# Kernel optimization log

Measured on AMD Instinct MI355X. Metric: run time of the kernel, lower is better.

Reference implementation:

```python
import jax, jax.numpy as jnp
import numpy as np

NF, NH, NC, B = 8, 200, 8, 131072  # nFeatures, nHidden, nCls, batch
NEQ = 2

def _lin_init(k, fan_in, fan_out):
    k1, k2 = jax.random.split(k)
    s = 1.0 / np.sqrt(fan_in)
    W = jax.random.uniform(k1, (fan_out, fan_in), minval=-s, maxval=s, dtype=jnp.float32)
    b = jax.random.uniform(k2, (fan_out,), minval=-s, maxval=s, dtype=jnp.float32)
    return W, b

def setup_inputs() -> dict:
    key = jax.random.key(0)
    ks = jax.random.split(key, 6)
    W0, b0 = _lin_init(ks[0], NF, NF)
    W1, b1 = _lin_init(ks[1], NF, NH)
    W2, b2 = _lin_init(ks[2], NH, NH)
    W3, b3 = _lin_init(ks[3], NH, NH)
    W4, b4 = _lin_init(ks[4], NH, NC)
    Q = jnp.eye(NF, dtype=jnp.float32)  # Parameter initialized to identity
    x = jax.random.normal(ks[5], (B, NF), dtype=jnp.float32)
    return dict(x=x, Q=Q, W0=W0, b0=b0, W1=W1, b1=b1, W2=W2, b2=b2, W3=W3, b3=b3, W4=W4, b4=b4)

def _qp_equality(Q, p, A, bvec):
    # min 1/2 z'Qz + p'z  s.t.  A z = b.  (G=0, h=0 => inequality constraints vacuous.)
    # KKT: [Q A'; A 0] [z; nu] = [-p; b], solved batched (tiny 10x10 systems).
    Bn, m, n = A.shape
    Qb = jnp.broadcast_to(Q, (Bn, n, n))
    K = jnp.concatenate([
        jnp.concatenate([Qb, jnp.swapaxes(A, 1, 2)], axis=2),        # [B, n, n+m]
        jnp.concatenate([A, jnp.zeros((Bn, m, m), Q.dtype)], axis=2) # [B, m, n+m]
    ], axis=1)                                                        # [B, n+m, n+m]
    rhs = jnp.concatenate([-p, bvec], axis=1)                         # [B, n+m]
    sol = jnp.linalg.solve(K, rhs[..., None])[..., 0]
    return sol[:, :n]

def reference(x, Q, W0, b0, W1, b1, W2, b2, W3, b3, W4, b4):
    h = x @ W0.T + b0                      # fc0, [B, 8]
    p = -h
    z_ = jnp.zeros_like(h[:, 3])
    o_ = jnp.ones_like(h[:, 3])
    # A[i] = [[0,0,0,0,h[i,3],1,0,0], [0,0,0,0,0,0,h[i,3],1]]  (detached in original)
    A = jnp.stack([
        jnp.stack([z_, z_, z_, z_, h[:, 3], o_, z_, z_], axis=1),
        jnp.stack([z_, z_, z_, z_, z_, z_, h[:, 3], o_], axis=1)], axis=1)  # [B, 2, 8]
    A = jax.lax.stop_gradient(A)  # torch.tensor(...) breaks the graph for A
    bvec = jnp.stack([h[:, 3] * h[:, 4] + h[:, 5],
                      h[:, 3] * h[:, 6] + h[:, 7]], axis=1)  # [B, 2]
    z = _qp_equality(Q, p, A, bvec)        # QPFunction solution, [B, 8]
    y = jax.nn.relu(z @ W1.T + b1)
    y = jax.nn.relu(y @ W2.T + b2)
    y = jax.nn.relu(y @ W3.T + b3)
    return y @ W4.T + b4                   # [B, 8]
```

## Files before the change

### kernel.cpp

```cpp
#include <hip/hip_runtime.h>
#include <math.h>

typedef _Float16 f16;
typedef f16 half8 __attribute__((ext_vector_type(8)));
typedef float floatx4 __attribute__((ext_vector_type(4)));

#define NF 8
#define NH 200
#define NC 8
#define M_BLK 256
#define SCR_W 40

#define WS_QI   0
#define WS_B1P  256
#define WS_B2P  1152
#define WS_B3P  2048
#define WS_WP1  3008
#define WS_WP2  16320
#define WS_WP3  109504
#define WS_WP4  202688
#define WS_NEED 209856

__device__ __forceinline__ void pack_frag(const float* __restrict__ W, int Nv, int Kv,
                                          int nkt, int nks, f16* __restrict__ dst, int gid)
{
    if (gid < nks * nkt * 64) {
        const int ks    = gid / (nkt * 64);
        const int rem   = gid - ks * nkt * 64;
        const int nt    = rem >> 6;
        const int lane  = rem & 63;
        const int n     = nt * 16 + (lane & 15);
        const int kbase = ks * 32 + ((lane >> 4) * 8);
        f16 tmp[8];
#pragma unroll
        for (int j = 0; j < 8; ++j) {
            const int k = kbase + j;
            tmp[j] = (n < Nv && k < Kv) ? (f16)W[n * Kv + k] : (f16)0.0f;
        }
        *(half8*)&dst[(size_t)gid * 8] = *(const half8*)tmp;
    }
}

__global__ void prep_kernel(const float* __restrict__ Q,
                            const float* __restrict__ W1, const float* __restrict__ b1,
                            const float* __restrict__ W2, const float* __restrict__ b2,
                            const float* __restrict__ W3, const float* __restrict__ b3,
                            const float* __restrict__ W4,
                            char* __restrict__ ws)
{
    const int gid = blockIdx.x * 256 + threadIdx.x;
    pack_frag(W1, NH, NF, 13, 1, (f16*)(ws + WS_WP1), gid);
    pack_frag(W2, NH, NH, 13, 7, (f16*)(ws + WS_WP2), gid);
    pack_frag(W3, NH, NH, 13, 7, (f16*)(ws + WS_WP3), gid);
    pack_frag(W4, NC, NH, 1,  7, (f16*)(ws + WS_WP4), gid);
    if (gid < 224) {
        ((float*)(ws + WS_B1P))[gid] = (gid < NH) ? b1[gid] : 0.0f;
        ((float*)(ws + WS_B2P))[gid] = (gid < NH) ? b2[gid] : 0.0f;
        ((float*)(ws + WS_B3P))[gid] = (gid < NH) ? b3[gid] : 0.0f;
    }

    if (blockIdx.x == 0) {
        __shared__ float aug[8][16];
        __shared__ int piv;
        float* Qi = (float*)(ws + WS_QI);
        const int t  = threadIdx.x;
        const bool a = t < 128;
        const int r  = (t >> 4) & 7;
        const int c2 = t & 15;
        if (a) aug[r][c2] = (c2 < 8) ? Q[r * 8 + c2] : ((c2 - 8 == r) ? 1.0f : 0.0f);
        __syncthreads();
        for (int c = 0; c < 8; ++c) {
            if (t == 0) {
                int p = c; float best = fabsf(aug[c][c]);
                for (int rr = c + 1; rr < 8; ++rr) {
                    float v = fabsf(aug[rr][c]);
                    if (v > best) { best = v; p = rr; }
                }
                piv = p;
            }
            __syncthreads();
            const int p = piv;
            float myv = a ? aug[r][c2] : 0.0f;
            __syncthreads();
            if (a) {
                if (r == c)      aug[p][c2] = myv;
                else if (r == p) aug[c][c2] = myv;
            }
            __syncthreads();
            const float pv = aug[c][c];
            __syncthreads();
            if (a && r == c) aug[r][c2] = aug[r][c2] / pv;
            __syncthreads();
            const float fac  = (a && r != c) ? aug[r][c] : 0.0f;
            const float prow = aug[c][c2];
            __syncthreads();
            if (a) aug[r][c2] -= fac * prow;
            __syncthreads();
        }
        if (a && c2 >= 8) Qi[r * 8 + (c2 - 8)] = aug[r][c2];
    }
}

template<int NKS>
__device__ __forceinline__ void layer_slab(const f16* __restrict__ Wp,
                                           const float* __restrict__ biasP,
                                           const half8 (&aIn)[4][7], half8 (&aOut)[4][7],
                                           f16* scr, const int lane,
                                           const int col16, const int g4)
{
#pragma unroll
    for (int p = 0; p < 7; ++p) {
        const int NT = (p < 6) ? 2 : 1;
        const float bv0 = biasP[(2 * p) * 16 + col16];
        const float bv1 = (NT == 2) ? biasP[(2 * p + 1) * 16 + col16] : 0.0f;
        floatx4 acc[4][2];
#pragma unroll
        for (int mt = 0; mt < 4; ++mt) {
            floatx4 v0; v0[0] = bv0; v0[1] = bv0; v0[2] = bv0; v0[3] = bv0;
            acc[mt][0] = v0;
            floatx4 v1; v1[0] = bv1; v1[1] = bv1; v1[2] = bv1; v1[3] = bv1;
            acc[mt][1] = v1;
        }
#pragma unroll
        for (int ks = 0; ks < NKS; ++ks) {
            const half8 bf0 = *(const half8*)&Wp[((size_t)(ks * 13 + 2 * p) * 64 + lane) * 8];
            half8 bf1;
            if (NT == 2) bf1 = *(const half8*)&Wp[((size_t)(ks * 13 + 2 * p + 1) * 64 + lane) * 8];
#pragma unroll
            for (int mt = 0; mt < 4; ++mt) {
                acc[mt][0] = __builtin_amdgcn_mfma_f32_16x16x32_f16(aIn[mt][ks], bf0, acc[mt][0], 0, 0, 0);
                if (NT == 2)
                    acc[mt][1] = __builtin_amdgcn_mfma_f32_16x16x32_f16(aIn[mt][ks], bf1, acc[mt][1], 0, 0, 0);
            }
        }
#pragma unroll
        for (int mt = 0; mt < 4; ++mt) {
#pragma unroll
            for (int r = 0; r < 4; ++r) {
                const int row = mt * 16 + g4 * 4 + r;
                scr[row * SCR_W + col16]      = (f16)fmaxf(acc[mt][0][r], 0.0f);
                if (NT == 2)
                    scr[row * SCR_W + 16 + col16] = (f16)fmaxf(acc[mt][1][r], 0.0f);
                else
                    scr[row * SCR_W + 16 + col16] = (f16)0.0f;
            }
        }
#pragma unroll
        for (int mt = 0; mt < 4; ++mt)
            aOut[mt][p] = *(const half8*)&scr[(mt * 16 + col16) * SCR_W + g4 * 8];
    }
}

__global__ __launch_bounds__(256, 1)
void mlp_slab(const float* __restrict__ x,
              const float* __restrict__ W0, const float* __restrict__ b0,
              const float* __restrict__ b4,
              const char* __restrict__ ws,
              float* __restrict__ out, int B)
{
    __shared__ f16 scrAll[4][64 * SCR_W];
    const int tid   = threadIdx.x;
    const int lane  = tid & 63;
    const int w     = __builtin_amdgcn_readfirstlane(tid >> 6);
    const int col16 = lane & 15;
    const int g4    = lane >> 4;
    f16* scr = &scrAll[w][0];

    const float* Qi  = (const float*)(ws + WS_QI);
    const float* b1p = (const float*)(ws + WS_B1P);
    const float* b2p = (const float*)(ws + WS_B2P);
    const float* b3p = (const float*)(ws + WS_B3P);
    const f16*  Wp1  = (const f16*)(ws + WS_WP1);
    const f16*  Wp2  = (const f16*)(ws + WS_WP2);
    const f16*  Wp3  = (const f16*)(ws + WS_WP3);
    const f16*  Wp4  = (const f16*)(ws + WS_WP4);

    const long g0 = (long)blockIdx.x * M_BLK + w * 64 + lane;
    float xr[NF];
    if (g0 < B) {
        const float4* xp = (const float4*)(x + g0 * NF);
        const float4 A = xp[0], Bv = xp[1];
        xr[0] = A.x; xr[1] = A.y; xr[2] = A.z; xr[3] = A.w;
        xr[4] = Bv.x; xr[5] = Bv.y; xr[6] = Bv.z; xr[7] = Bv.w;
    } else {
#pragma unroll
        for (int i = 0; i < NF; ++i) xr[i] = 0.0f;
    }
    float h[NF];
#pragma unroll
    for (int j = 0; j < NF; ++j) {
        float acc = b0[j];
#pragma unroll
        for (int k = 0; k < NF; ++k) acc = fmaf(W0[j * NF + k], xr[k], acc);
        h[j] = acc;
    }
    float tq[NF], u0[NF], u1[NF];
    const float h3 = h[3];
#pragma unroll
    for (int i = 0; i < NF; ++i) {
        float s = 0.0f;
#pragma unroll
        for (int k = 0; k < NF; ++k) s = fmaf(Qi[i * NF + k], h[k], s);
        tq[i] = s;
        u0[i] = fmaf(Qi[i * NF + 4], h3, Qi[i * NF + 5]);
        u1[i] = fmaf(Qi[i * NF + 6], h3, Qi[i * NF + 7]);
    }
    const float m00 = fmaf(h3, u0[4], u0[5]);
    const float m01 = fmaf(h3, u1[4], u1[5]);
    const float m10 = fmaf(h3, u0[6], u0[7]);
    const float m11 = fmaf(h3, u1[6], u1[7]);
    const float r0  = fmaf(h3, tq[4], tq[5]) - fmaf(h3, h[4], h[5]);
    const float r1  = fmaf(h3, tq[6], tq[7]) - fmaf(h3, h[6], h[7]);
    const float idet = 1.0f / (m00 * m11 - m01 * m10);
    const float nu0 = (m11 * r0 - m01 * r1) * idet;
    const float nu1 = (m00 * r1 - m10 * r0) * idet;

    {
        half8 zh, zz = {};
#pragma unroll
        for (int k = 0; k < 8; ++k) zh[k] = (f16)(tq[k] - u0[k] * nu0 - u1[k] * nu1);
        *(half8*)&scr[lane * SCR_W + 0]  = zh;
        *(half8*)&scr[lane * SCR_W + 8]  = zz;
        *(half8*)&scr[lane * SCR_W + 16] = zz;
        *(half8*)&scr[lane * SCR_W + 24] = zz;
    }

    half8 aA[4][7], aB[4][7];
#pragma unroll
    for (int mt = 0; mt < 4; ++mt)
        aA[mt][0] = *(const half8*)&scr[(mt * 16 + col16) * SCR_W + g4 * 8];

    layer_slab<1>(Wp1, b1p, aA, aB, scr, lane, col16, g4);
    layer_slab<7>(Wp2, b2p, aB, aA, scr, lane, col16, g4);
    layer_slab<7>(Wp3, b3p, aA, aB, scr, lane, col16, g4);

    {
        const float bias4 = b4[col16 & 7];
        floatx4 acc4[4];
#pragma unroll
        for (int mt = 0; mt < 4; ++mt) { floatx4 z_ = {}; acc4[mt] = z_; }
#pragma unroll
        for (int ks = 0; ks < 7; ++ks) {
            const half8 bf = *(const half8*)&Wp4[((size_t)ks * 64 + lane) * 8];
#pragma unroll
            for (int mt = 0; mt < 4; ++mt)
                acc4[mt] = __builtin_amdgcn_mfma_f32_16x16x32_f16(aB[mt][ks], bf, acc4[mt], 0, 0, 0);
        }
        const long rowbase = (long)blockIdx.x * M_BLK + w * 64;
#pragma unroll
        for (int mt = 0; mt < 4; ++mt) {
#pragma unroll
            for (int r = 0; r < 4; ++r) {
                const long g = rowbase + mt * 16 + g4 * 4 + r;
                if (col16 < NC && g < B) out[g * NC + col16] = acc4[mt][r] + bias4;
            }
        }
    }
}

#define BT 64
#define NWAVE 8
#define JB 25
#define CH 8

__device__ __forceinline__ void layer200(const float* __restrict__ in_,
                                         float* __restrict__ out_,
                                         const float* __restrict__ W,
                                         const float* __restrict__ bias,
                                         int j0, int lane)
{
    float acc[JB];
#pragma unroll
    for (int jj = 0; jj < JB; ++jj) acc[jj] = bias[j0 + jj];
#pragma unroll 1
    for (int k0 = 0; k0 < NH; k0 += CH) {
        float a[CH];
#pragma unroll
        for (int u = 0; u < CH; ++u) a[u] = in_[(k0 + u) * BT + lane];
#pragma unroll
        for (int jj = 0; jj < JB; ++jj) {
            const float* wr = W + (j0 + jj) * NH + k0;
#pragma unroll
            for (int u = 0; u < CH; ++u) acc[jj] = fmaf(wr[u], a[u], acc[jj]);
        }
    }
#pragma unroll
    for (int jj = 0; jj < JB; ++jj)
        out_[(j0 + jj) * BT + lane] = fmaxf(acc[jj], 0.0f);
}

__global__ void qinv_kernel(const float* __restrict__ Q, float* __restrict__ Qi)
{
    __shared__ float aug[8][16];
    __shared__ int piv;
    const int t  = threadIdx.x;
    const int r  = t >> 4;
    const int c2 = t & 15;
    aug[r][c2] = (c2 < 8) ? Q[r * 8 + c2] : ((c2 - 8 == r) ? 1.0f : 0.0f);
    __syncthreads();
    for (int c = 0; c < 8; ++c) {
        if (t == 0) {
            int p = c; float best = fabsf(aug[c][c]);
            for (int rr = c + 1; rr < 8; ++rr) {
                float v = fabsf(aug[rr][c]);
                if (v > best) { best = v; p = rr; }
            }
            piv = p;
        }
        __syncthreads();
        const int p = piv;
        float myv = aug[r][c2];
        __syncthreads();
        if (r == c)      aug[p][c2] = myv;
        else if (r == p) aug[c][c2] = myv;
        __syncthreads();
        const float pv = aug[c][c];
        __syncthreads();
        if (r == c) aug[r][c2] = aug[r][c2] / pv;
        __syncthreads();
        const float fac  = (r == c) ? 0.0f : aug[r][c];
        const float prow = aug[c][c2];
        __syncthreads();
        aug[r][c2] -= fac * prow;
        __syncthreads();
    }
    if (c2 >= 8) Qi[r * 8 + (c2 - 8)] = aug[r][c2];
}

__global__ __launch_bounds__(BT * NWAVE, 2)
void mlp_fused(const float* __restrict__ x, const float* __restrict__ Qi,
               const float* __restrict__ W0, const float* __restrict__ b0,
               const float* __restrict__ W1, const float* __restrict__ b1,
               const float* __restrict__ W2, const float* __restrict__ b2,
               const float* __restrict__ W3, const float* __restrict__ b3,
               const float* __restrict__ W4, const float* __restrict__ b4,
               float* __restrict__ out, int B)
{
    __shared__ float actA[NH * BT];
    __shared__ float actB[NH * BT];
    __shared__ float outP[NWAVE * NC * BT];

    const int lane = threadIdx.x & 63;
    const int wid  = __builtin_amdgcn_readfirstlane((int)(threadIdx.x >> 6));
    const int g    = blockIdx.x * BT + lane;
    const int j0   = wid * JB;

    float xr[NF];
    if (g < B) {
        const float4* xp = reinterpret_cast<const float4*>(x + (size_t)g * NF);
        float4 x0 = xp[0], x1 = xp[1];
        xr[0] = x0.x; xr[1] = x0.y; xr[2] = x0.z; xr[3] = x0.w;
        xr[4] = x1.x; xr[5] = x1.y; xr[6] = x1.z; xr[7] = x1.w;
    } else {
#pragma unroll
        for (int i = 0; i < NF; ++i) xr[i] = 0.0f;
    }
    float h[NF];
#pragma unroll
    for (int j = 0; j < NF; ++j) {
        float acc = b0[j];
#pragma unroll
        for (int k = 0; k < NF; ++k) acc = fmaf(W0[j * NF + k], xr[k], acc);
        h[j] = acc;
    }
    float tq[NF], u0[NF], u1[NF];
    const float h3 = h[3];
#pragma unroll
    for (int i = 0; i < NF; ++i) {
        float s = 0.0f;
#pragma unroll
        for (int k = 0; k < NF; ++k) s = fmaf(Qi[i * NF + k], h[k], s);
        tq[i] = s;
        u0[i] = fmaf(Qi[i * NF + 4], h3, Qi[i * NF + 5]);
        u1[i] = fmaf(Qi[i * NF + 6], h3, Qi[i * NF + 7]);
    }
    const float m00 = fmaf(h3, u0[4], u0[5]);
    const float m01 = fmaf(h3, u1[4], u1[5]);
    const float m10 = fmaf(h3, u0[6], u0[7]);
    const float m11 = fmaf(h3, u1[6], u1[7]);
    const float r0  = fmaf(h3, tq[4], tq[5]) - fmaf(h3, h[4], h[5]);
    const float r1  = fmaf(h3, tq[6], tq[7]) - fmaf(h3, h[6], h[7]);
    const float idet = 1.0f / (m00 * m11 - m01 * m10);
    const float nu0 = (m11 * r0 - m01 * r1) * idet;
    const float nu1 = (m00 * r1 - m10 * r0) * idet;
    float z[NF];
#pragma unroll
    for (int i = 0; i < NF; ++i) z[i] = tq[i] - u0[i] * nu0 - u1[i] * nu1;

#pragma unroll
    for (int jj = 0; jj < JB; ++jj) {
        const int j = j0 + jj;
        float acc = b1[j];
#pragma unroll
        for (int k = 0; k < NF; ++k) acc = fmaf(W1[j * NF + k], z[k], acc);
        actA[j * BT + lane] = fmaxf(acc, 0.0f);
    }
    __syncthreads();
    layer200(actA, actB, W2, b2, j0, lane);
    __syncthreads();
    layer200(actB, actA, W3, b3, j0, lane);
    __syncthreads();
    {
        float a[JB];
#pragma unroll
        for (int kk = 0; kk < JB; ++kk) a[kk] = actA[(j0 + kk) * BT + lane];
        float acc[NC];
#pragma unroll
        for (int o = 0; o < NC; ++o) acc[o] = 0.0f;
#pragma unroll
        for (int o = 0; o < NC; ++o) {
            const float* wr = W4 + o * NH + j0;
#pragma unroll
            for (int kk = 0; kk < JB; ++kk) acc[o] = fmaf(wr[kk], a[kk], acc[o]);
        }
#pragma unroll
        for (int o = 0; o < NC; ++o) outP[(wid * NC + o) * BT + lane] = acc[o];
    }
    __syncthreads();
    {
        float s = b4[wid];
#pragma unroll
        for (int w = 0; w < NWAVE; ++w) s += outP[(w * NC + wid) * BT + lane];
        if (g < B) out[(size_t)g * NC + wid] = s;
    }
}

extern "C" void kernel_launch(void* const* d_in, const int* in_sizes, int n_in,
                              void* d_out, int out_size, void* d_ws, size_t ws_size,
                              hipStream_t stream)
{
    const float* x  = (const float*)d_in[0];
    const float* Q  = (const float*)d_in[1];
    const float* W0 = (const float*)d_in[2];
    const float* b0 = (const float*)d_in[3];
    const float* W1 = (const float*)d_in[4];
    const float* b1 = (const float*)d_in[5];
    const float* W2 = (const float*)d_in[6];
    const float* b2 = (const float*)d_in[7];
    const float* W3 = (const float*)d_in[8];
    const float* b3 = (const float*)d_in[9];
    const float* W4 = (const float*)d_in[10];
    const float* b4 = (const float*)d_in[11];
    float* out = (float*)d_out;

    const int B = in_sizes[0] / NF;

    if (ws_size >= WS_NEED) {
        hipLaunchKernelGGL(prep_kernel, dim3(23), dim3(256), 0, stream,
                           Q, W1, b1, W2, b2, W3, b3, W4, (char*)d_ws);
        hipLaunchKernelGGL(mlp_slab, dim3((B + M_BLK - 1) / M_BLK), dim3(256), 0, stream,
                           x, W0, b0, b4, (const char*)d_ws, out, B);
    } else {
        float* Qi = (float*)d_ws;
        hipLaunchKernelGGL(qinv_kernel, dim3(1), dim3(128), 0, stream, Q, Qi);
        hipLaunchKernelGGL(mlp_fused, dim3((B + BT - 1) / BT), dim3(BT * NWAVE), 0, stream,
                           x, Qi, W0, b0, W1, b1, W2, b2, W3, b3, W4, b4, out, B);
    }
}
```

Measured before the change: 52.74 us.

## Transpose MFMA tiling so weights are the A operand, with register shuffles instead of LDS

Replaces the 256-thread, 4-wave slab kernel with a single-wave kernel that handles 48 rows per block. It computes W·actᵀ so the weight fragments become the MFMA A operand and activations stay in registers. The LDS round trip between layers is replaced by packed fp16 conversion and cross-lane shuffles, and outputs are written as float4. The intent is to remove LDS traffic and barriers, but it adds many more blocks. Each 48-row tile also re-reads all weight fragments from global memory, and a quarter of the MFMA columns in the 64-lane layout are wasted.

New measurement: 60.13 us. 1.14x slower.

```diff
diff --git a/kernel.cpp b/kernel.cpp
--- a/kernel.cpp
+++ b/kernel.cpp
@@ -8,8 +8,8 @@
 #define NF 8
 #define NH 200
 #define NC 8
-#define M_BLK 256
-#define SCR_W 40
+#define ROWS_T 48
+#define FRAG 512
 
 #define WS_QI   0
 #define WS_B1P  256
@@ -19,7 +19,7 @@
 #define WS_WP2  16320
 #define WS_WP3  109504
 #define WS_WP4  202688
-#define WS_NEED 209856
+#define WS_NEED 212000
 
 __device__ __forceinline__ void pack_frag(const float* __restrict__ W, int Nv, int Kv,
                                           int nkt, int nks, f16* __restrict__ dst, int gid)
@@ -101,70 +101,111 @@
     }
 }
 
-template<int NKS>
-__device__ __forceinline__ void layer_slab(const f16* __restrict__ Wp,
-                                           const float* __restrict__ biasP,
-                                           const half8 (&aIn)[4][7], half8 (&aOut)[4][7],
-                                           f16* scr, const int lane,
-                                           const int col16, const int g4)
-{
-#pragma unroll
-    for (int p = 0; p < 7; ++p) {
-        const int NT = (p < 6) ? 2 : 1;
-        const float bv0 = biasP[(2 * p) * 16 + col16];
-        const float bv1 = (NT == 2) ? biasP[(2 * p + 1) * 16 + col16] : 0.0f;
-        floatx4 acc[4][2];
-#pragma unroll
-        for (int mt = 0; mt < 4; ++mt) {
-            floatx4 v0; v0[0] = bv0; v0[1] = bv0; v0[2] = bv0; v0[3] = bv0;
-            acc[mt][0] = v0;
-            floatx4 v1; v1[0] = bv1; v1[1] = bv1; v1[2] = bv1; v1[3] = bv1;
-            acc[mt][1] = v1;
-        }
-#pragma unroll
-        for (int ks = 0; ks < NKS; ++ks) {
-            const half8 bf0 = *(const half8*)&Wp[((size_t)(ks * 13 + 2 * p) * 64 + lane) * 8];
-            half8 bf1;
-            if (NT == 2) bf1 = *(const half8*)&Wp[((size_t)(ks * 13 + 2 * p + 1) * 64 + lane) * 8];
-#pragma unroll
-            for (int mt = 0; mt < 4; ++mt) {
-                acc[mt][0] = __builtin_amdgcn_mfma_f32_16x16x32_f16(aIn[mt][ks], bf0, acc[mt][0], 0, 0, 0);
-                if (NT == 2)
-                    acc[mt][1] = __builtin_amdgcn_mfma_f32_16x16x32_f16(aIn[mt][ks], bf1, acc[mt][1], 0, 0, 0);
-            }
-        }
-#pragma unroll
-        for (int mt = 0; mt < 4; ++mt) {
-#pragma unroll
-            for (int r = 0; r < 4; ++r) {
-                const int row = mt * 16 + g4 * 4 + r;
-                scr[row * SCR_W + col16]      = (f16)fmaxf(acc[mt][0][r], 0.0f);
-                if (NT == 2)
-                    scr[row * SCR_W + 16 + col16] = (f16)fmaxf(acc[mt][1][r], 0.0f);
-                else
-                    scr[row * SCR_W + 16 + col16] = (f16)0.0f;
-            }
-        }
-#pragma unroll
-        for (int mt = 0; mt < 4; ++mt)
-            aOut[mt][p] = *(const half8*)&scr[(mt * 16 + col16) * SCR_W + g4 * 8];
-    }
-}
-
-__global__ __launch_bounds__(256, 1)
-void mlp_slab(const float* __restrict__ x,
-              const float* __restrict__ W0, const float* __restrict__ b0,
-              const float* __restrict__ b4,
-              const char* __restrict__ ws,
-              float* __restrict__ out, int B)
-{
-    __shared__ f16 scrAll[4][64 * SCR_W];
-    const int tid   = threadIdx.x;
-    const int lane  = tid & 63;
-    const int w     = __builtin_amdgcn_readfirstlane(tid >> 6);
-    const int col16 = lane & 15;
-    const int g4    = lane >> 4;
-    f16* scr = &scrAll[w][0];
+__device__ __forceinline__ half8 ldf(const f16* __restrict__ p, int lane)
+{
+    return *(const half8*)&p[lane * 8];
+}
+
+__device__ __forceinline__ int pk2(float a, float b)
+{
+    typedef __fp16 hv2 __attribute__((ext_vector_type(2)));
+    hv2 h = __builtin_amdgcn_cvt_pkrtz(a, b);
+    int r; __builtin_memcpy(&r, &h, 4);
+    return r;
+}
+
+__device__ __forceinline__ half8 mk8(int a, int b, int c, int d)
+{
+    int v[4] = {a, b, c, d};
+    half8 h; __builtin_memcpy(&h, v, 16);
+    return h;
+}
+
+template<int LK>
+__device__ __forceinline__ void layerT(const f16* __restrict__ Wp,
+                                       const float* __restrict__ biasP,
+                                       const half8 (&act)[3][7], half8 (&nxt)[3][7],
+                                       const int lane, const int g,
+                                       const int se, const int so)
+{
+#pragma unroll
+    for (int w = 0; w < 7; ++w) {
+        const int mA = 2 * w;
+        floatx4 accA[3];
+        {
+            half8 wfA[LK];
+#pragma unroll
+            for (int ks = 0; ks < LK; ++ks)
+                wfA[ks] = ldf(Wp + (size_t)(ks * 13 + mA) * FRAG, lane);
+            const float4 bv = *(const float4*)&biasP[mA * 16 + 4 * g];
+#pragma unroll
+            for (int n = 0; n < 3; ++n) {
+                accA[n][0] = bv.x; accA[n][1] = bv.y; accA[n][2] = bv.z; accA[n][3] = bv.w;
+            }
+#pragma unroll
+            for (int ks = 0; ks < LK; ++ks)
+#pragma unroll
+                for (int n = 0; n < 3; ++n)
+                    accA[n] = __builtin_amdgcn_mfma_f32_16x16x32_f16(
+                        wfA[ks], act[n][ks], accA[n], 0, 0, 0);
+        }
+        if (w < 6) {
+            const int mB = mA + 1;
+            floatx4 accB[3];
+            half8 wfB[LK];
+#pragma unroll
+            for (int ks = 0; ks < LK; ++ks)
+                wfB[ks] = ldf(Wp + (size_t)(ks * 13 + mB) * FRAG, lane);
+            const float4 bv = *(const float4*)&biasP[mB * 16 + 4 * g];
+#pragma unroll
+            for (int n = 0; n < 3; ++n) {
+                accB[n][0] = bv.x; accB[n][1] = bv.y; accB[n][2] = bv.z; accB[n][3] = bv.w;
+            }
+#pragma unroll
+            for (int ks = 0; ks < LK; ++ks)
+#pragma unroll
+                for (int n = 0; n < 3; ++n)
+                    accB[n] = __builtin_amdgcn_mfma_f32_16x16x32_f16(
+                        wfB[ks], act[n][ks], accB[n], 0, 0, 0);
+#pragma unroll
+            for (int n = 0; n < 3; ++n) {
+                const int a0 = pk2(fmaxf(accA[n][0], 0.0f), fmaxf(accA[n][1], 0.0f));
+                const int a1 = pk2(fmaxf(accA[n][2], 0.0f), fmaxf(accA[n][3], 0.0f));
+                const int b0 = pk2(fmaxf(accB[n][0], 0.0f), fmaxf(accB[n][1], 0.0f));
+                const int b1 = pk2(fmaxf(accB[n][2], 0.0f), fmaxf(accB[n][3], 0.0f));
+                const int tA0 = __shfl(a0, se, 64), tA1 = __shfl(a1, se, 64);
+                const int tA2 = __shfl(a0, so, 64), tA3 = __shfl(a1, so, 64);
+                const int tB0 = __shfl(b0, se, 64), tB1 = __shfl(b1, se, 64);
+                const int tB2 = __shfl(b0, so, 64), tB3 = __shfl(b1, so, 64);
+                nxt[n][w] = mk8((g < 2) ? tA0 : tB0, (g < 2) ? tA1 : tB1,
+                                (g < 2) ? tA2 : tB2, (g < 2) ? tA3 : tB3);
+            }
+        } else {
+#pragma unroll
+            for (int n = 0; n < 3; ++n) {
+                const int a0 = pk2(fmaxf(accA[n][0], 0.0f), fmaxf(accA[n][1], 0.0f));
+                const int a1 = pk2(fmaxf(accA[n][2], 0.0f), fmaxf(accA[n][3], 0.0f));
+                const int tA0 = __shfl(a0, se, 64), tA1 = __shfl(a1, se, 64);
+                const int tA2 = __shfl(a0, so, 64), tA3 = __shfl(a1, so, 64);
+                nxt[n][w] = mk8((g < 2) ? tA0 : 0, (g < 2) ? tA1 : 0,
+                                (g < 2) ? tA2 : 0, (g < 2) ? tA3 : 0);
+            }
+        }
+    }
+}
+
+__global__ __launch_bounds__(64, 2)
+void mlp_t(const float* __restrict__ x,
+           const float* __restrict__ W0, const float* __restrict__ b0,
+           const float* __restrict__ b4,
+           const char* __restrict__ ws,
+           float* __restrict__ out, int B)
+{
+    const int lane = threadIdx.x & 63;
+    const int c    = lane & 15;
+    const int g    = lane >> 4;
+    const int se   = ((2 * g) & 3) * 16 + c;
+    const int so   = se + 16;
 
     const float* Qi  = (const float*)(ws + WS_QI);
     const float* b1p = (const float*)(ws + WS_B1P);
@@ -175,9 +216,9 @@
     const f16*  Wp3  = (const f16*)(ws + WS_WP3);
     const f16*  Wp4  = (const f16*)(ws + WS_WP4);
 
-    const long g0 = (long)blockIdx.x * M_BLK + w * 64 + lane;
+    const long g0 = (long)blockIdx.x * ROWS_T + lane;
     float xr[NF];
-    if (g0 < B) {
+    if (lane < ROWS_T && g0 < B) {
         const float4* xp = (const float4*)(x + g0 * NF);
         const float4 A = xp[0], Bv = xp[1];
         xr[0] = A.x; xr[1] = A.y; xr[2] = A.z; xr[3] = A.w;
@@ -214,45 +255,55 @@
     const float idet = 1.0f / (m00 * m11 - m01 * m10);
     const float nu0 = (m11 * r0 - m01 * r1) * idet;
     const float nu1 = (m00 * r1 - m10 * r0) * idet;
+    float z[NF];
+#pragma unroll
+    for (int i = 0; i < NF; ++i) z[i] = tq[i] - u0[i] * nu0 - u1[i] * nu1;
+
+    int zq[4];
+#pragma unroll
+    for (int j = 0; j < 4; ++j) zq[j] = pk2(z[2 * j], z[2 * j + 1]);
+
+    half8 aA[3][7], aB[3][7];
+#pragma unroll
+    for (int n = 0; n < 3; ++n) {
+        const int src = 16 * n + c;
+        const int q0 = __shfl(zq[0], src, 64), q1 = __shfl(zq[1], src, 64);
+        const int q2 = __shfl(zq[2], src, 64), q3 = __shfl(zq[3], src, 64);
+        aA[n][0] = mk8((g == 0) ? q0 : 0, (g == 0) ? q1 : 0,
+                       (g == 0) ? q2 : 0, (g == 0) ? q3 : 0);
+    }
+
+    layerT<1>(Wp1, b1p, aA, aB, lane, g, se, so);
+    layerT<7>(Wp2, b2p, aB, aA, lane, g, se, so);
+    layerT<7>(Wp3, b3p, aA, aB, lane, g, se, so);
 
     {
-        half8 zh, zz = {};
-#pragma unroll
-        for (int k = 0; k < 8; ++k) zh[k] = (f16)(tq[k] - u0[k] * nu0 - u1[k] * nu1);
-        *(half8*)&scr[lane * SCR_W + 0]  = zh;
-        *(half8*)&scr[lane * SCR_W + 8]  = zz;
-        *(half8*)&scr[lane * SCR_W + 16] = zz;
-        *(half8*)&scr[lane * SCR_W + 24] = zz;
-    }
-
-    half8 aA[4][7], aB[4][7];
-#pragma unroll
-    for (int mt = 0; mt < 4; ++mt)
-        aA[mt][0] = *(const half8*)&scr[(mt * 16 + col16) * SCR_W + g4 * 8];
-
-    layer_slab<1>(Wp1, b1p, aA, aB, scr, lane, col16, g4);
-    layer_slab<7>(Wp2, b2p, aB, aA, scr, lane, col16, g4);
-    layer_slab<7>(Wp3, b3p, aA, aB, scr, lane, col16, g4);
-
-    {
-        const float bias4 = b4[col16 & 7];
-        floatx4 acc4[4];
-#pragma unroll
-        for (int mt = 0; mt < 4; ++mt) { floatx4 z_ = {}; acc4[mt] = z_; }
-#pragma unroll
-        for (int ks = 0; ks < 7; ++ks) {
-            const half8 bf = *(const half8*)&Wp4[((size_t)ks * 64 + lane) * 8];
-#pragma unroll
-            for (int mt = 0; mt < 4; ++mt)
-                acc4[mt] = __builtin_amdgcn_mfma_f32_16x16x32_f16(aB[mt][ks], bf, acc4[mt], 0, 0, 0);
-        }
-        const long rowbase = (long)blockIdx.x * M_BLK + w * 64;
-#pragma unroll
-        for (int mt = 0; mt < 4; ++mt) {
-#pragma unroll
-            for (int r = 0; r < 4; ++r) {
-                const long g = rowbase + mt * 16 + g4 * 4 + r;
-                if (col16 < NC && g < B) out[g * NC + col16] = acc4[mt][r] + bias4;
+        floatx4 a4[3];
+        const int boff = (g < 2) ? 4 * g : 0;
+        const float4 bv = *(const float4*)&b4[boff];
+#pragma unroll
+        for (int n = 0; n < 3; ++n) {
+            a4[n][0] = bv.x; a4[n][1] = bv.y; a4[n][2] = bv.z; a4[n][3] = bv.w;
+        }
+        half8 wf4[7];
+#pragma unroll
+        for (int ks = 0; ks < 7; ++ks) wf4[ks] = ldf(Wp4 + (size_t)ks * FRAG, lane);
+#pragma unroll
+        for (int ks = 0; ks < 7; ++ks)
+#pragma unroll
+            for (int n = 0; n < 3; ++n)
+                a4[n] = __builtin_amdgcn_mfma_f32_16x16x32_f16(
+                    wf4[ks], aB[n][ks], a4[n], 0, 0, 0);
+        if (g < 2) {
+            const long rowbase = (long)blockIdx.x * ROWS_T;
+#pragma unroll
+            for (int n = 0; n < 3; ++n) {
+                const long row = rowbase + 16 * n + c;
+                if (row < B) {
+                    float4 v;
+                    v.x = a4[n][0]; v.y = a4[n][1]; v.z = a4[n][2]; v.w = a4[n][3];
+                    *(float4*)&out[row * NC + 4 * g] = v;
+                }
             }
         }
     }
@@ -448,7 +499,7 @@
     if (ws_size >= WS_NEED) {
         hipLaunchKernelGGL(prep_kernel, dim3(23), dim3(256), 0, stream,
                            Q, W1, b1, W2, b2, W3, b3, W4, (char*)d_ws);
-        hipLaunchKernelGGL(mlp_slab, dim3((B + M_BLK - 1) / M_BLK), dim3(256), 0, stream,
+        hipLaunchKernelGGL(mlp_t, dim3((B + ROWS_T - 1) / ROWS_T), dim3(64), 0, stream,
                            x, W0, b0, b4, (const char*)d_ws, out, B);
     } else {
         float* Qi = (float*)d_ws;
```

## Hold weight fragments in registers and split output columns across waves

Applied to the files above, without the earlier changes.

The slab kernel, where each wave streamed every weight fragment for its own 64 rows, becomes a 512-thread kernel in which each of 8 waves keeps a fixed subset of output-column tiles' weight fragments resident in registers. Activations for 128-row chunks pass between layers through shared memory, and each block loops over 4 chunks while prefetching the next chunk's x. The goal is to stop reloading weights from global/L2 for every row tile. The cost is many block-wide syncs per layer, larger LDS use, high register pressure, and partial-sum reduction for the last layer through shared memory.

Result: faster. 50.61 us (-4.0%).

```diff
diff --git a/kernel.cpp b/kernel.cpp
--- a/kernel.cpp
+++ b/kernel.cpp
@@ -8,8 +8,11 @@
 #define NF 8
 #define NH 200
 #define NC 8
-#define M_BLK 256
-#define SCR_W 40
+#define ACT_W 232
+#define ROWS 128
+#define CHUNK 4
+#define OUTP_W 9
+#define FRAG 512
 
 #define WS_QI   0
 #define WS_B1P  256
@@ -19,7 +22,7 @@
 #define WS_WP2  16320
 #define WS_WP3  109504
 #define WS_WP4  202688
-#define WS_NEED 209856
+#define WS_NEED 212000
 
 __device__ __forceinline__ void pack_frag(const float* __restrict__ W, int Nv, int Kv,
                                           int nkt, int nks, f16* __restrict__ dst, int gid)
@@ -101,71 +104,22 @@
     }
 }
 
-template<int NKS>
-__device__ __forceinline__ void layer_slab(const f16* __restrict__ Wp,
-                                           const float* __restrict__ biasP,
-                                           const half8 (&aIn)[4][7], half8 (&aOut)[4][7],
-                                           f16* scr, const int lane,
-                                           const int col16, const int g4)
-{
-#pragma unroll
-    for (int p = 0; p < 7; ++p) {
-        const int NT = (p < 6) ? 2 : 1;
-        const float bv0 = biasP[(2 * p) * 16 + col16];
-        const float bv1 = (NT == 2) ? biasP[(2 * p + 1) * 16 + col16] : 0.0f;
-        floatx4 acc[4][2];
-#pragma unroll
-        for (int mt = 0; mt < 4; ++mt) {
-            floatx4 v0; v0[0] = bv0; v0[1] = bv0; v0[2] = bv0; v0[3] = bv0;
-            acc[mt][0] = v0;
-            floatx4 v1; v1[0] = bv1; v1[1] = bv1; v1[2] = bv1; v1[3] = bv1;
-            acc[mt][1] = v1;
-        }
-#pragma unroll
-        for (int ks = 0; ks < NKS; ++ks) {
-            const half8 bf0 = *(const half8*)&Wp[((size_t)(ks * 13 + 2 * p) * 64 + lane) * 8];
-            half8 bf1;
-            if (NT == 2) bf1 = *(const half8*)&Wp[((size_t)(ks * 13 + 2 * p + 1) * 64 + lane) * 8];
-#pragma unroll
-            for (int mt = 0; mt < 4; ++mt) {
-                acc[mt][0] = __builtin_amdgcn_mfma_f32_16x16x32_f16(aIn[mt][ks], bf0, acc[mt][0], 0, 0, 0);
-                if (NT == 2)
-                    acc[mt][1] = __builtin_amdgcn_mfma_f32_16x16x32_f16(aIn[mt][ks], bf1, acc[mt][1], 0, 0, 0);
-            }
-        }
-#pragma unroll
-        for (int mt = 0; mt < 4; ++mt) {
-#pragma unroll
-            for (int r = 0; r < 4; ++r) {
-                const int row = mt * 16 + g4 * 4 + r;
-                scr[row * SCR_W + col16]      = (f16)fmaxf(acc[mt][0][r], 0.0f);
-                if (NT == 2)
-                    scr[row * SCR_W + 16 + col16] = (f16)fmaxf(acc[mt][1][r], 0.0f);
-                else
-                    scr[row * SCR_W + 16 + col16] = (f16)0.0f;
-            }
-        }
-#pragma unroll
-        for (int mt = 0; mt < 4; ++mt)
-            aOut[mt][p] = *(const half8*)&scr[(mt * 16 + col16) * SCR_W + g4 * 8];
-    }
-}
-
-__global__ __launch_bounds__(256, 1)
-void mlp_slab(const float* __restrict__ x,
-              const float* __restrict__ W0, const float* __restrict__ b0,
-              const float* __restrict__ b4,
-              const char* __restrict__ ws,
-              float* __restrict__ out, int B)
-{
-    __shared__ f16 scrAll[4][64 * SCR_W];
-    const int tid   = threadIdx.x;
-    const int lane  = tid & 63;
-    const int w     = __builtin_amdgcn_readfirstlane(tid >> 6);
-    const int col16 = lane & 15;
-    const int g4    = lane >> 4;
-    f16* scr = &scrAll[w][0];
-
+__device__ __forceinline__ half8 ldf(const f16* __restrict__ p, int lane)
+{
+    return *(const half8*)&p[lane * 8];
+}
+
+template<int TC>
+__device__ __forceinline__ void run_path(
+    const float* __restrict__ x,
+    const float* __restrict__ W0, const float* __restrict__ b0,
+    const float* __restrict__ b4,
+    const char* __restrict__ ws,
+    float* __restrict__ out, int B,
+    f16* __restrict__ actA, f16* __restrict__ actB,
+    f16* __restrict__ zbuf, float* __restrict__ outP,
+    const int wid, const int lane, const int c, const int g, const int t0)
+{
     const float* Qi  = (const float*)(ws + WS_QI);
     const float* b1p = (const float*)(ws + WS_B1P);
     const float* b2p = (const float*)(ws + WS_B2P);
@@ -175,87 +129,222 @@
     const f16*  Wp3  = (const f16*)(ws + WS_WP3);
     const f16*  Wp4  = (const f16*)(ws + WS_WP4);
 
-    const long g0 = (long)blockIdx.x * M_BLK + w * 64 + lane;
+    half8 wf1[TC], wf2[TC][7], wf3[TC][7];
+    float bv1[TC], bv2[TC], bv3[TC];
+#pragma unroll
+    for (int t = 0; t < TC; ++t) {
+        wf1[t] = ldf(Wp1 + (size_t)(t0 + t) * FRAG, lane);
+#pragma unroll
+        for (int ks = 0; ks < 7; ++ks) {
+            wf2[t][ks] = ldf(Wp2 + (size_t)(ks * 13 + t0 + t) * FRAG, lane);
+            wf3[t][ks] = ldf(Wp3 + (size_t)(ks * 13 + t0 + t) * FRAG, lane);
+        }
+        bv1[t] = b1p[(t0 + t) * 16 + c];
+        bv2[t] = b2p[(t0 + t) * 16 + c];
+        bv3[t] = b3p[(t0 + t) * 16 + c];
+    }
+    const bool doL4 = (wid < 7);
+    half8 w4f = {};
+    if (doL4) w4f = ldf(Wp4 + (size_t)wid * FRAG, lane);
+
+    const long blockbase = (long)blockIdx.x * (ROWS * CHUNK);
+    const int  tid = wid * 64 + lane;
+
+    {
+        f16* buf = (tid & 256) ? actB : actA;
+        const int row  = (tid >> 1) & 127;
+        const int part = tid & 1;
+        half8 zz = {};
+        *(half8*)&buf[row * ACT_W + 208 + part * 8] = zz;
+    }
+
     float xr[NF];
-    if (g0 < B) {
-        const float4* xp = (const float4*)(x + g0 * NF);
-        const float4 A = xp[0], Bv = xp[1];
-        xr[0] = A.x; xr[1] = A.y; xr[2] = A.z; xr[3] = A.w;
-        xr[4] = Bv.x; xr[5] = Bv.y; xr[6] = Bv.z; xr[7] = Bv.w;
-    } else {
-#pragma unroll
-        for (int i = 0; i < NF; ++i) xr[i] = 0.0f;
-    }
-    float h[NF];
-#pragma unroll
-    for (int j = 0; j < NF; ++j) {
-        float acc = b0[j];
-#pragma unroll
-        for (int k = 0; k < NF; ++k) acc = fmaf(W0[j * NF + k], xr[k], acc);
-        h[j] = acc;
-    }
-    float tq[NF], u0[NF], u1[NF];
-    const float h3 = h[3];
-#pragma unroll
-    for (int i = 0; i < NF; ++i) {
-        float s = 0.0f;
-#pragma unroll
-        for (int k = 0; k < NF; ++k) s = fmaf(Qi[i * NF + k], h[k], s);
-        tq[i] = s;
-        u0[i] = fmaf(Qi[i * NF + 4], h3, Qi[i * NF + 5]);
-        u1[i] = fmaf(Qi[i * NF + 6], h3, Qi[i * NF + 7]);
-    }
-    const float m00 = fmaf(h3, u0[4], u0[5]);
-    const float m01 = fmaf(h3, u1[4], u1[5]);
-    const float m10 = fmaf(h3, u0[6], u0[7]);
-    const float m11 = fmaf(h3, u1[6], u1[7]);
-    const float r0  = fmaf(h3, tq[4], tq[5]) - fmaf(h3, h[4], h[5]);
-    const float r1  = fmaf(h3, tq[6], tq[7]) - fmaf(h3, h[6], h[7]);
-    const float idet = 1.0f / (m00 * m11 - m01 * m10);
-    const float nu0 = (m11 * r0 - m01 * r1) * idet;
-    const float nu1 = (m00 * r1 - m10 * r0) * idet;
-
-    {
-        half8 zh, zz = {};
-#pragma unroll
-        for (int k = 0; k < 8; ++k) zh[k] = (f16)(tq[k] - u0[k] * nu0 - u1[k] * nu1);
-        *(half8*)&scr[lane * SCR_W + 0]  = zh;
-        *(half8*)&scr[lane * SCR_W + 8]  = zz;
-        *(half8*)&scr[lane * SCR_W + 16] = zz;
-        *(half8*)&scr[lane * SCR_W + 24] = zz;
-    }
-
-    half8 aA[4][7], aB[4][7];
-#pragma unroll
-    for (int mt = 0; mt < 4; ++mt)
-        aA[mt][0] = *(const half8*)&scr[(mt * 16 + col16) * SCR_W + g4 * 8];
-
-    layer_slab<1>(Wp1, b1p, aA, aB, scr, lane, col16, g4);
-    layer_slab<7>(Wp2, b2p, aB, aA, scr, lane, col16, g4);
-    layer_slab<7>(Wp3, b3p, aA, aB, scr, lane, col16, g4);
-
-    {
-        const float bias4 = b4[col16 & 7];
-        floatx4 acc4[4];
-#pragma unroll
-        for (int mt = 0; mt < 4; ++mt) { floatx4 z_ = {}; acc4[mt] = z_; }
-#pragma unroll
-        for (int ks = 0; ks < 7; ++ks) {
-            const half8 bf = *(const half8*)&Wp4[((size_t)ks * 64 + lane) * 8];
-#pragma unroll
-            for (int mt = 0; mt < 4; ++mt)
-                acc4[mt] = __builtin_amdgcn_mfma_f32_16x16x32_f16(aB[mt][ks], bf, acc4[mt], 0, 0, 0);
-        }
-        const long rowbase = (long)blockIdx.x * M_BLK + w * 64;
-#pragma unroll
-        for (int mt = 0; mt < 4; ++mt) {
-#pragma unroll
-            for (int r = 0; r < 4; ++r) {
-                const long g = rowbase + mt * 16 + g4 * 4 + r;
-                if (col16 < NC && g < B) out[g * NC + col16] = acc4[mt][r] + bias4;
-            }
-        }
-    }
+    const int hrow = wid * 64 + lane;
+#pragma unroll
+    for (int i = 0; i < NF; ++i) xr[i] = 0.0f;
+    if (wid < 2) {
+        const long gr = blockbase + hrow;
+        if (gr < B) {
+            const float4* xp = (const float4*)(x + gr * NF);
+            const float4 A = xp[0], Bv = xp[1];
+            xr[0] = A.x; xr[1] = A.y; xr[2] = A.z; xr[3] = A.w;
+            xr[4] = Bv.x; xr[5] = Bv.y; xr[6] = Bv.z; xr[7] = Bv.w;
+        }
+    }
+
+#pragma unroll 1
+    for (int ck = 0; ck < CHUNK; ++ck) {
+        const long base = blockbase + (long)ck * ROWS;
+
+        if (wid < 2) {
+            float xn[NF];
+#pragma unroll
+            for (int i = 0; i < NF; ++i) xn[i] = 0.0f;
+            if (ck + 1 < CHUNK) {
+                const long gn = base + ROWS + hrow;
+                if (gn < B) {
+                    const float4* xp = (const float4*)(x + gn * NF);
+                    const float4 A = xp[0], Bv = xp[1];
+                    xn[0] = A.x; xn[1] = A.y; xn[2] = A.z; xn[3] = A.w;
+                    xn[4] = Bv.x; xn[5] = Bv.y; xn[6] = Bv.z; xn[7] = Bv.w;
+                }
+            }
+            float h[NF];
+#pragma unroll
+            for (int j = 0; j < NF; ++j) {
+                float acc = b0[j];
+#pragma unroll
+                for (int k = 0; k < NF; ++k) acc = fmaf(W0[j * NF + k], xr[k], acc);
+                h[j] = acc;
+            }
+            float tq[NF], u0[NF], u1[NF];
+            const float h3 = h[3];
+#pragma unroll
+            for (int i = 0; i < NF; ++i) {
+                float s = 0.0f;
+#pragma unroll
+                for (int k = 0; k < NF; ++k) s = fmaf(Qi[i * NF + k], h[k], s);
+                tq[i] = s;
+                u0[i] = fmaf(Qi[i * NF + 4], h3, Qi[i * NF + 5]);
+                u1[i] = fmaf(Qi[i * NF + 6], h3, Qi[i * NF + 7]);
+            }
+            const float m00 = fmaf(h3, u0[4], u0[5]);
+            const float m01 = fmaf(h3, u1[4], u1[5]);
+            const float m10 = fmaf(h3, u0[6], u0[7]);
+            const float m11 = fmaf(h3, u1[6], u1[7]);
+            const float r0  = fmaf(h3, tq[4], tq[5]) - fmaf(h3, h[4], h[5]);
+            const float r1  = fmaf(h3, tq[6], tq[7]) - fmaf(h3, h[6], h[7]);
+            const float idet = 1.0f / (m00 * m11 - m01 * m10);
+            const float nu0 = (m11 * r0 - m01 * r1) * idet;
+            const float nu1 = (m00 * r1 - m10 * r0) * idet;
+            half8 zh, zz = {};
+#pragma unroll
+            for (int k = 0; k < 8; ++k) zh[k] = (f16)(tq[k] - u0[k] * nu0 - u1[k] * nu1);
+            *(half8*)&zbuf[hrow * 32 + 0]  = zh;
+            *(half8*)&zbuf[hrow * 32 + 8]  = zz;
+            *(half8*)&zbuf[hrow * 32 + 16] = zz;
+            *(half8*)&zbuf[hrow * 32 + 24] = zz;
+#pragma unroll
+            for (int i = 0; i < NF; ++i) xr[i] = xn[i];
+        }
+        __syncthreads();
+
+#pragma unroll
+        for (int m = 0; m < 8; ++m) {
+            const half8 az = *(const half8*)&zbuf[(m * 16 + c) * 32 + g * 8];
+#pragma unroll
+            for (int t = 0; t < TC; ++t) {
+                floatx4 acc;
+                acc[0] = bv1[t]; acc[1] = bv1[t]; acc[2] = bv1[t]; acc[3] = bv1[t];
+                acc = __builtin_amdgcn_mfma_f32_16x16x32_f16(az, wf1[t], acc, 0, 0, 0);
+#pragma unroll
+                for (int r = 0; r < 4; ++r)
+                    actA[(m * 16 + g * 4 + r) * ACT_W + (t0 + t) * 16 + c] =
+                        (f16)fmaxf(acc[r], 0.0f);
+            }
+        }
+        __syncthreads();
+
+#pragma unroll
+        for (int m = 0; m < 8; ++m) {
+            half8 af[7];
+#pragma unroll
+            for (int ks = 0; ks < 7; ++ks)
+                af[ks] = *(const half8*)&actA[(m * 16 + c) * ACT_W + ks * 32 + g * 8];
+#pragma unroll
+            for (int t = 0; t < TC; ++t) {
+                floatx4 acc;
+                acc[0] = bv2[t]; acc[1] = bv2[t]; acc[2] = bv2[t]; acc[3] = bv2[t];
+#pragma unroll
+                for (int ks = 0; ks < 7; ++ks)
+                    acc = __builtin_amdgcn_mfma_f32_16x16x32_f16(af[ks], wf2[t][ks], acc, 0, 0, 0);
+#pragma unroll
+                for (int r = 0; r < 4; ++r)
+                    actB[(m * 16 + g * 4 + r) * ACT_W + (t0 + t) * 16 + c] =
+                        (f16)fmaxf(acc[r], 0.0f);
+            }
+        }
+        __syncthreads();
+
+#pragma unroll
+        for (int m = 0; m < 8; ++m) {
+            half8 af[7];
+#pragma unroll
+            for (int ks = 0; ks < 7; ++ks)
+                af[ks] = *(const half8*)&actB[(m * 16 + c) * ACT_W + ks * 32 + g * 8];
+#pragma unroll
+            for (int t = 0; t < TC; ++t) {
+                floatx4 acc;
+                acc[0] = bv3[t]; acc[1] = bv3[t]; acc[2] = bv3[t]; acc[3] = bv3[t];
+#pragma unroll
+                for (int ks = 0; ks < 7; ++ks)
+                    acc = __builtin_amdgcn_mfma_f32_16x16x32_f16(af[ks], wf3[t][ks], acc, 0, 0, 0);
+#pragma unroll
+                for (int r = 0; r < 4; ++r)
+                    actA[(m * 16 + g * 4 + r) * ACT_W + (t0 + t) * 16 + c] =
+                        (f16)fmaxf(acc[r], 0.0f);
+            }
+        }
+        __syncthreads();
+
+        if (doL4) {
+#pragma unroll
+            for (int m = 0; m < 8; ++m) {
+                const half8 af = *(const half8*)&actA[(m * 16 + c) * ACT_W + wid * 32 + g * 8];
+                floatx4 a4 = {};
+                a4 = __builtin_amdgcn_mfma_f32_16x16x32_f16(af, w4f, a4, 0, 0, 0);
+                if (c < NC) {
+#pragma unroll
+                    for (int r = 0; r < 4; ++r)
+                        outP[(wid * ROWS + m * 16 + g * 4 + r) * OUTP_W + c] = a4[r];
+                }
+            }
+        }
+        __syncthreads();
+
+        {
+            const int e   = tid * 2;
+            const int row = e >> 3;
+            const int col = e & 7;
+            float s0 = b4[col], s1 = b4[col + 1];
+#pragma unroll
+            for (int w = 0; w < 7; ++w) {
+                s0 += outP[(w * ROWS + row) * OUTP_W + col];
+                s1 += outP[(w * ROWS + row) * OUTP_W + col + 1];
+            }
+            const long gr = base + row;
+            if (gr < B) {
+                float2 v; v.x = s0; v.y = s1;
+                *(float2*)&out[gr * NC + col] = v;
+            }
+        }
+    }
+}
+
+__global__ __launch_bounds__(512, 2)
+void mlp_pers(const float* __restrict__ x,
+              const float* __restrict__ W0, const float* __restrict__ b0,
+              const float* __restrict__ b4,
+              const char* __restrict__ ws,
+              float* __restrict__ out, int B)
+{
+    __shared__ f16   actA[ROWS * ACT_W];
+    __shared__ f16   actB[ROWS * ACT_W];
+    __shared__ f16   zbuf[ROWS * 32];
+    __shared__ float outP[7 * ROWS * OUTP_W];
+
+    const int tid  = threadIdx.x;
+    const int lane = tid & 63;
+    const int wid  = __builtin_amdgcn_readfirstlane(tid >> 6);
+    const int c    = lane & 15;
+    const int g    = lane >> 4;
+
+    if (wid < 5)
+        run_path<2>(x, W0, b0, b4, ws, out, B, actA, actB, zbuf, outP,
+                    wid, lane, c, g, 2 * wid);
+    else
+        run_path<1>(x, W0, b0, b4, ws, out, B, actA, actB, zbuf, outP,
+                    wid, lane, c, g, wid + 5);
 }
 
 #define BT 64
@@ -448,7 +537,8 @@
     if (ws_size >= WS_NEED) {
         hipLaunchKernelGGL(prep_kernel, dim3(23), dim3(256), 0, stream,
                            Q, W1, b1, W2, b2, W3, b3, W4, (char*)d_ws);
-        hipLaunchKernelGGL(mlp_slab, dim3((B + M_BLK - 1) / M_BLK), dim3(256), 0, stream,
+        const int nblk = (B + ROWS * CHUNK - 1) / (ROWS * CHUNK);
+        hipLaunchKernelGGL(mlp_pers, dim3(nblk), dim3(512), 0, stream,
                            x, W0, b0, b4, (const char*)d_ws, out, B);
     } else {
         float* Qi = (float*)d_ws;
```
